# Performance work log

Measured on AMD Instinct MI355X. Metric: run time of the kernel, lower is better.

## Reference

```python
import jax, jax.numpy as jnp
import numpy as np

ALPHA = 0.0
# tetra edge vertex pairs, same order as the original: (0,1),(0,2),(0,3),(1,2),(1,3),(2,3)
EDGE_PAIRS = np.array([[0, 1], [0, 2], [0, 3], [1, 2], [1, 3], [2, 3]], dtype=np.int32)


def setup_inputs() -> dict:
    key = jax.random.key(0)
    B, N, T = 2, 120000, 600000
    k1, k2 = jax.random.split(key)
    pred = jax.random.normal(k1, (B, N, 4), dtype=jnp.float32)
    tetra = jax.random.randint(k2, (B, T, 4), 0, N, dtype=jnp.int32)
    return {"pred": pred, "tetra": tetra}


def _laplace_tetra(verts, faces):
    # verts: [N,4], faces: [T,4] int. For vertex slot j, contribution is
    # sum_{k != j} (v_k - v_j) = (v0+v1+v2+v3) - 4*v_j ; weight 3 per incidence.
    N = verts.shape[0]
    v = verts[faces]                                  # [T,4,4]
    vsum = jnp.sum(v, axis=1, keepdims=True)          # [T,1,4]
    contrib = (vsum - 4.0 * v).reshape(-1, 4)         # [T*4,4]
    idx = faces.reshape(-1)
    term = jax.ops.segment_sum(contrib, idx, num_segments=N)
    norm = jax.ops.segment_sum(jnp.full(idx.shape, 3.0, verts.dtype), idx, num_segments=N)
    term = term / jnp.clip(norm, 1.0)[:, None]
    return jnp.mean(term ** 2)


def reference(pred, tetra):
    tetra = tetra.astype(jnp.int32)
    # center pred over the point dimension (axis=1)
    pred = pred - jnp.mean(pred, axis=1, keepdims=True)

    def per_batch(pre, tetr):
        L1 = _laplace_tetra(pre, tetr)
        Tetrah = pre[tetr]                             # [T,4,4]
        pa = Tetrah[:, EDGE_PAIRS[:, 0], :]            # [T,6,4] edge endpoint 0
        pb = Tetrah[:, EDGE_PAIRS[:, 1], :]            # [T,6,4] edge endpoint 1
        wa = pa[..., 3]
        wb = pb[..., 3]
        edge = (wa - ALPHA) * (wb - ALPHA)             # [T,6]
        L2 = jnp.mean(wa * wb)
        L3 = jnp.mean((jnp.linalg.norm(pa - pb, axis=-1) - 0.4) ** 2)
        # zero-crossing interpolation: x = (alpha - w0)*m/q + x0
        d = pa - pb                                    # [T,6,4]
        q = d[..., 3]
        safe_q = jnp.where(jnp.abs(q) > 1e-12, q, 1.0)
        t = (ALPHA - wa) / safe_q                      # [T,6]
        pts = pa[..., :3] + t[..., None] * d[..., :3]  # [T,6,3]
        mask = edge < 0                                # valid crossing edges
        pts = jnp.where(mask[..., None], pts, 0.0)
        return L1, L2, L3, pts, mask

    L1, L2, L3, pts, mask = jax.vmap(per_batch)(pred, tetra)
    # losses = [L1, L2, L3, L4] (L4 is always 0 in the original)
    losses = jnp.stack([jnp.mean(L1), jnp.mean(L2), jnp.mean(L3), jnp.zeros((), pred.dtype)])
    return losses, pts, mask
```

## Files before the change

### kernel.cpp

```cpp
#include <hip/hip_runtime.h>


#define VPB 2048
#define VPB_SHIFT 11
#define KMAX 120
#define LAP_M 8
#define CAP 49152u
#define FP_BIAS 16.0f
#define FP_SCALE 8.0f
#define FP_INV   0.125f
#define FMASK 0x3FFFULL

typedef float vf4  __attribute__((ext_vector_type(4)));
typedef float vf4u __attribute__((ext_vector_type(4), aligned(4)));
typedef int   vi4  __attribute__((ext_vector_type(4)));

__device__ inline double waveReduce(double v) {
    #pragma unroll
    for (int off = 32; off > 0; off >>= 1) v += __shfl_down(v, off);
    return v;
}

__device__ inline void block_copy_nt(float* __restrict__ dst,
                                     const float* __restrict__ src, int n) {
    int n4 = n >> 2;
    const vf4* s4 = (const vf4*)src;
    vf4u* d4 = (vf4u*)dst;
    for (int i = threadIdx.x; i < n4; i += 256) {
        vf4u v = s4[i];
        __builtin_nontemporal_store(v, d4 + i);
    }
    for (int i = (n4 << 2) + threadIdx.x; i < n; i += 256)
        dst[i] = src[i];
}

__device__ inline void block_copy_u8_nt(float* __restrict__ dst,
                                        const unsigned char* __restrict__ src,
                                        int n) {
    int n4 = n >> 2;
    const uchar4* s4 = (const uchar4*)src;
    vf4u* d4 = (vf4u*)dst;
    for (int i = threadIdx.x; i < n4; i += 256) {
        uchar4 c = s4[i];
        vf4u v = { (float)c.x, (float)c.y, (float)c.z, (float)c.w };
        __builtin_nontemporal_store(v, d4 + i);
    }
    for (int i = (n4 << 2) + threadIdx.x; i < n; i += 256)
        dst[i] = (float)src[i];
}

__global__ __launch_bounds__(256) void mean_kernel(
    const float* __restrict__ pred, double* __restrict__ mpart,
    unsigned* __restrict__ cursors, int N)
{
    if (blockIdx.x == 0 && blockIdx.y == 0 && threadIdx.x < KMAX)
        cursors[threadIdx.x] = 0u;

    const int b = blockIdx.y;
    const float4* p = (const float4*)pred + (size_t)b * N;
    double s0 = 0, s1 = 0, s2 = 0, s3 = 0;
    for (int n = blockIdx.x * blockDim.x + threadIdx.x; n < N;
         n += gridDim.x * blockDim.x) {
        float4 v = p[n];
        s0 += v.x; s1 += v.y; s2 += v.z; s3 += v.w;
    }
    s0 = waveReduce(s0); s1 = waveReduce(s1);
    s2 = waveReduce(s2); s3 = waveReduce(s3);
    __shared__ double mr[4][4];
    int wv = threadIdx.x >> 6;
    if ((threadIdx.x & 63) == 0) {
        mr[wv][0] = s0; mr[wv][1] = s1; mr[wv][2] = s2; mr[wv][3] = s3;
    }
    __syncthreads();
    if (threadIdx.x < 4) {
        double a = mr[0][threadIdx.x] + mr[1][threadIdx.x]
                 + mr[2][threadIdx.x] + mr[3][threadIdx.x];
        mpart[((size_t)b * 32 + blockIdx.x) * 4 + threadIdx.x] = a;
    }
}

__device__ inline void edge_phase(const float4* vr,
                                  float m0, float m1, float m2, float m3,
                                  double& l2, double& l3,
                                  float* lds_pts, unsigned char* lds_msk)
{
    float4 v[4];
    #pragma unroll
    for (int s = 0; s < 4; s++)
        v[s] = make_float4(vr[s].x - m0, vr[s].y - m1, vr[s].z - m2, vr[s].w - m3);
    const int EA[6] = {0, 0, 0, 1, 1, 2};
    const int EB[6] = {1, 2, 3, 2, 3, 3};
    #pragma unroll
    for (int e = 0; e < 6; e++) {
        float4 pa = v[EA[e]], pb = v[EB[e]];
        float wa = pa.w, wb = pb.w;
        float edge = wa * wb;
        float dx = pa.x - pb.x, dy = pa.y - pb.y;
        float dz = pa.z - pb.z, dw = pa.w - pb.w;
        l2 += (double)edge;
        float nr = sqrtf(dx * dx + dy * dy + dz * dz + dw * dw) - 0.4f;
        l3 += (double)(nr * nr);
        float sq = (fabsf(dw) > 1e-12f) ? dw : 1.0f;
        float tt = (0.0f - wa) / sq;
        bool msk = edge < 0.0f;
        lds_pts[threadIdx.x * 18 + e * 3 + 0] = msk ? (pa.x + tt * dx) : 0.0f;
        lds_pts[threadIdx.x * 18 + e * 3 + 1] = msk ? (pa.y + tt * dy) : 0.0f;
        lds_pts[threadIdx.x * 18 + e * 3 + 2] = msk ? (pa.z + tt * dz) : 0.0f;
        lds_msk[threadIdx.x * 6 + e] = msk ? 1 : 0;
    }
}

__device__ inline unsigned long long pack_rec(const float4* vr) {
    float sx = vr[0].x + vr[1].x + vr[2].x + vr[3].x;
    float sy = vr[0].y + vr[1].y + vr[2].y + vr[3].y;
    float sz = vr[0].z + vr[1].z + vr[2].z + vr[3].z;
    float sw = vr[0].w + vr[1].w + vr[2].w + vr[3].w;
    unsigned long long qx = (unsigned long long)((sx + FP_BIAS) * FP_SCALE + 0.5f);
    unsigned long long qy = (unsigned long long)((sy + FP_BIAS) * FP_SCALE + 0.5f);
    unsigned long long qz = (unsigned long long)((sz + FP_BIAS) * FP_SCALE + 0.5f);
    unsigned long long qw = (unsigned long long)((sw + FP_BIAS) * FP_SCALE + 0.5f);
    return qx | (qy << 9) | (qz << 18) | (qw << 27);
}

__device__ inline unsigned long long pack_ab(const float4* vr) {
    float sx = vr[0].x + vr[1].x + vr[2].x + vr[3].x;
    float sy = vr[0].y + vr[1].y + vr[2].y + vr[3].y;
    float sz = vr[0].z + vr[1].z + vr[2].z + vr[3].z;
    float sw = vr[0].w + vr[1].w + vr[2].w + vr[3].w;
    unsigned long long qx = (unsigned long long)((sx + FP_BIAS) * FP_SCALE + 0.5f);
    unsigned long long qy = (unsigned long long)((sy + FP_BIAS) * FP_SCALE + 0.5f);
    unsigned long long qz = (unsigned long long)((sz + FP_BIAS) * FP_SCALE + 0.5f);
    unsigned long long qw = (unsigned long long)((sw + FP_BIAS) * FP_SCALE + 0.5f);
    return qx | (qy << 14) | (qz << 28) | (qw << 42) | (1ULL << 56);
}

__global__ __launch_bounds__(256) void fused_kernel(
    const float* __restrict__ pred, const int* __restrict__ tetra,
    const double* __restrict__ mpart,
    unsigned long long* __restrict__ seg,
    unsigned* __restrict__ cursors,
    unsigned long long* __restrict__ AB,
    double* __restrict__ l2p, double* __restrict__ l3p,
    float* __restrict__ out, int N, int T, int B, int K, int mode)
{
    __shared__ __align__(16) float lds_pts[256 * 18];
    __shared__ __align__(16) unsigned char lds_msk[256 * 6];
    __shared__ double sr[2][4];
    __shared__ unsigned hist[KMAX];
    __shared__ unsigned basei[KMAX];
    __shared__ float bm[4];

    const int b = blockIdx.y;

    if (threadIdx.x < KMAX) hist[threadIdx.x] = 0;
    if (threadIdx.x < 4) {
        double s = 0.0;
        #pragma unroll
        for (int j = 0; j < 32; j++)
            s += mpart[((size_t)b * 32 + j) * 4 + threadIdx.x];
        bm[threadIdx.x] = (float)(s / N);
    }
    __syncthreads();

    const int tbase = blockIdx.x * 512;
    const int t0 = tbase + threadIdx.x;
    const int t1 = tbase + 256 + threadIdx.x;
    const bool v0 = (t0 < T), v1 = (t1 < T);
    float m0 = bm[0], m1 = bm[1], m2 = bm[2], m3 = bm[3];

    double l2 = 0.0, l3 = 0.0;
    int via[4] = {0,0,0,0}, vib[4] = {0,0,0,0};
    unsigned rnka[4] = {0,0,0,0}, rnkb[4] = {0,0,0,0};
    float4 vra[4], vrb[4];
    unsigned long long recq0 = 0, recq1 = 0;

    if (v0) {
        vi4 q = __builtin_nontemporal_load((const vi4*)tetra + (size_t)b * T + t0);
        via[0] = q.x; via[1] = q.y; via[2] = q.z; via[3] = q.w;
        #pragma unroll
        for (int s = 0; s < 4; s++)
            vra[s] = ((const float4*)pred)[(size_t)b * N + via[s]];
    }
    if (v1) {
        vi4 q = __builtin_nontemporal_load((const vi4*)tetra + (size_t)b * T + t1);
        vib[0] = q.x; vib[1] = q.y; vib[2] = q.z; vib[3] = q.w;
        #pragma unroll
        for (int s = 0; s < 4; s++)
            vrb[s] = ((const float4*)pred)[(size_t)b * N + vib[s]];
    }

    if (mode == 1) {
        if (v0) {
            #pragma unroll
            for (int s = 0; s < 4; s++) {
                unsigned gid = (unsigned)(b * N + via[s]);
                rnka[s] = atomicAdd(&hist[gid >> VPB_SHIFT], 1u);
            }
        }
        if (v1) {
            #pragma unroll
            for (int s = 0; s < 4; s++) {
                unsigned gid = (unsigned)(b * N + vib[s]);
                rnkb[s] = atomicAdd(&hist[gid >> VPB_SHIFT], 1u);
            }
        }
    }

    if (v0) {
        recq0 = (mode == 1) ? pack_rec(vra) : pack_ab(vra);
        edge_phase(vra, m0, m1, m2, m3, l2, l3, lds_pts, lds_msk);
    }
    __syncthreads();

    if (mode == 1 && threadIdx.x < K) {
        unsigned h = hist[threadIdx.x];
        basei[threadIdx.x] = h ? atomicAdd(&cursors[threadIdx.x], h) : 0u;
    }

    const int nv0 = min(256, T - tbase);
    {
        size_t pbase = 4 + ((size_t)b * T + tbase) * 18;
        block_copy_nt(out + pbase, lds_pts, nv0 * 18);
        size_t mbase = 4 + (size_t)B * T * 18 + ((size_t)b * T + tbase) * 6;
        block_copy_u8_nt(out + mbase, lds_msk, nv0 * 6);
    }
    __syncthreads();

    if (v1) {
        recq1 = (mode == 1) ? pack_rec(vrb) : pack_ab(vrb);
        edge_phase(vrb, m0, m1, m2, m3, l2, l3, lds_pts, lds_msk);
    }
    l2 = waveReduce(l2); l3 = waveReduce(l3);
    int wv = threadIdx.x >> 6;
    if ((threadIdx.x & 63) == 0) { sr[0][wv] = l2; sr[1][wv] = l3; }
    __syncthreads();

    const int nv1 = min(256, T - tbase - 256);
    if (nv1 > 0) {
        size_t pbase = 4 + ((size_t)b * T + tbase + 256) * 18;
        block_copy_nt(out + pbase, lds_pts, nv1 * 18);
        size_t mbase = 4 + (size_t)B * T * 18 + ((size_t)b * T + tbase + 256) * 6;
        block_copy_u8_nt(out + mbase, lds_msk, nv1 * 6);
    }

    if (threadIdx.x == 0) {
        double a = 0, c = 0;
        #pragma unroll
        for (int w = 0; w < 4; w++) { a += sr[0][w]; c += sr[1][w]; }
        int blk = blockIdx.y * gridDim.x + blockIdx.x;
        l2p[blk] = a;
        l3p[blk] = c;
    }

    if (mode == 1) {
        if (v0) {
            #pragma unroll
            for (int s = 0; s < 4; s++) {
                unsigned gid = (unsigned)(b * N + via[s]);
                unsigned bk = gid >> VPB_SHIFT;
                unsigned slot = basei[bk] + rnka[s];
                if (slot < CAP)
                    seg[(size_t)bk * CAP + slot] =
                        recq0 | ((unsigned long long)(gid & (VPB - 1)) << 36);
            }
        }
        if (v1) {
            #pragma unroll
            for (int s = 0; s < 4; s++) {
                unsigned gid = (unsigned)(b * N + vib[s]);
                unsigned bk = gid >> VPB_SHIFT;
                unsigned slot = basei[bk] + rnkb[s];
                if (slot < CAP)
                    seg[(size_t)bk * CAP + slot] =
                        recq1 | ((unsigned long long)(gid & (VPB - 1)) << 36);
            }
        }
    } else {
        if (v0) {
            #pragma unroll
            for (int s = 0; s < 4; s++)
                atomicAdd(&AB[(size_t)b * N + via[s]], recq0);
        }
        if (v1) {
            #pragma unroll
            for (int s = 0; s < 4; s++)
                atomicAdd(&AB[(size_t)b * N + vib[s]], recq1);
        }
    }
}

__device__ inline unsigned long long rec_decode(unsigned long long r) {
    return (r & 511ULL)
         | (((r >> 9)  & 511ULL) << 14)
         | (((r >> 18) & 511ULL) << 28)
         | (((r >> 27) & 511ULL) << 42)
         | (1ULL << 56);
}

__global__ __launch_bounds__(256) void lap1_kernel(
    const unsigned long long* __restrict__ seg,
    const unsigned* __restrict__ cursors,
    unsigned long long* __restrict__ partial, int M)
{
    __shared__ unsigned long long acc[VPB];
    const int bkt = blockIdx.x;
    const int m = blockIdx.y;

    for (int i = threadIdx.x; i < VPB; i += 256) acc[i] = 0ULL;
    __syncthreads();

    unsigned cnt = min(cursors[bkt], CAP);
    unsigned per = (cnt + M - 1) / M;
    unsigned lo = m * per;
    unsigned hi = min(cnt, lo + per);
    const unsigned long long* s0 = seg + (size_t)bkt * CAP;

    unsigned i = lo + threadIdx.x;
    for (; i + 768 < hi; i += 1024) {
        unsigned long long r0 = __builtin_nontemporal_load(&s0[i]);
        unsigned long long r1 = __builtin_nontemporal_load(&s0[i + 256]);
        unsigned long long r2 = __builtin_nontemporal_load(&s0[i + 512]);
        unsigned long long r3 = __builtin_nontemporal_load(&s0[i + 768]);
        atomicAdd(&acc[(unsigned)(r0 >> 36) & (VPB - 1)], rec_decode(r0));
        atomicAdd(&acc[(unsigned)(r1 >> 36) & (VPB - 1)], rec_decode(r1));
        atomicAdd(&acc[(unsigned)(r2 >> 36) & (VPB - 1)], rec_decode(r2));
        atomicAdd(&acc[(unsigned)(r3 >> 36) & (VPB - 1)], rec_decode(r3));
    }
    for (; i < hi; i += 256) {
        unsigned long long r = __builtin_nontemporal_load(&s0[i]);
        atomicAdd(&acc[(unsigned)(r >> 36) & (VPB - 1)], rec_decode(r));
    }
    __syncthreads();

    unsigned long long* p = partial + ((size_t)bkt * M + m) * VPB;
    for (int i2 = threadIdx.x; i2 < VPB; i2 += 256) p[i2] = acc[i2];
}

__global__ __launch_bounds__(256) void lap2_kernel(
    const unsigned long long* __restrict__ partial,
    const float* __restrict__ pred, double* __restrict__ l1p, int BN, int M)
{
    int gid = blockIdx.x * 256 + threadIdx.x;
    double s = 0.0;
    if (gid < BN) {
        int bkt = gid >> VPB_SHIFT;
        int rel = gid & (VPB - 1);
        const unsigned long long* p =
            partial + (size_t)bkt * M * VPB + rel;
        unsigned long long P = 0;
        #pragma unroll 4
        for (int m = 0; m < M; m++) P += p[(size_t)m * VPB];
        int c = (int)(P >> 56);
        float cb = (float)c * FP_BIAS;
        float Sx = (float)(unsigned)( P        & FMASK) * FP_INV - cb;
        float Sy = (float)(unsigned)((P >> 14) & FMASK) * FP_INV - cb;
        float Sz = (float)(unsigned)((P >> 28) & FMASK) * FP_INV - cb;
        float Sw = (float)(unsigned)((P >> 42) & FMASK) * FP_INV - cb;
        float4 v = ((const float4*)pred)[gid];
        float fc = 4.0f * (float)c;
        float tx = Sx - fc * v.x, ty = Sy - fc * v.y;
        float tz = Sz - fc * v.z, tw = Sw - fc * v.w;
        float dn = fmaxf(3.0f * (float)c, 1.0f);
        tx /= dn; ty /= dn; tz /= dn; tw /= dn;
        s = (double)(tx * tx) + (double)(ty * ty)
          + (double)(tz * tz) + (double)(tw * tw);
    }
    s = waveReduce(s);
    __shared__ double sr[4];
    int wv = threadIdx.x >> 6;
    if ((threadIdx.x & 63) == 0) sr[wv] = s;
    __syncthreads();
    if (threadIdx.x == 0) {
        double a = 0;
        #pragma unroll
        for (int w = 0; w < 4; w++) a += sr[w];
        l1p[blockIdx.x] = a;
    }
}

__global__ __launch_bounds__(256) void l1_kernel(
    const unsigned long long* __restrict__ AB, const float* __restrict__ pred,
    double* __restrict__ l1p, int BN)
{
    int i = blockIdx.x * 256 + threadIdx.x;
    double s = 0.0;
    if (i < BN) {
        unsigned long long P = AB[i];
        int c = (int)(P >> 56);
        float cb = (float)c * FP_BIAS;
        float Sx = (float)(unsigned)( P        & FMASK) * FP_INV - cb;
        float Sy = (float)(unsigned)((P >> 14) & FMASK) * FP_INV - cb;
        float Sz = (float)(unsigned)((P >> 28) & FMASK) * FP_INV - cb;
        float Sw = (float)(unsigned)((P >> 42) & FMASK) * FP_INV - cb;
        float4 v = ((const float4*)pred)[i];
        float fc = 4.0f * (float)c;
        float tx = Sx - fc * v.x, ty = Sy - fc * v.y;
        float tz = Sz - fc * v.z, tw = Sw - fc * v.w;
        float dn = fmaxf(3.0f * (float)c, 1.0f);
        tx /= dn; ty /= dn; tz /= dn; tw /= dn;
        s = (double)(tx * tx) + (double)(ty * ty)
          + (double)(tz * tz) + (double)(tw * tw);
    }
    s = waveReduce(s);
    __shared__ double sr[4];
    int wv = threadIdx.x >> 6;
    if ((threadIdx.x & 63) == 0) sr[wv] = s;
    __syncthreads();
    if (threadIdx.x == 0) {
        double a = 0;
        #pragma unroll
        for (int w = 0; w < 4; w++) a += sr[w];
        l1p[blockIdx.x] = a;
    }
}

__global__ __launch_bounds__(256) void finalize_kernel(
    const double* __restrict__ l1p, const double* __restrict__ l2p,
    const double* __restrict__ l3p, float* __restrict__ out,
    double nd1, double nd23, int n1, int n23)
{
    double s1 = 0, s2 = 0, s3 = 0;
    for (int i = threadIdx.x; i < n23; i += 256) { s2 += l2p[i]; s3 += l3p[i]; }
    for (int i = threadIdx.x; i < n1; i += 256) s1 += l1p[i];
    s1 = waveReduce(s1); s2 = waveReduce(s2); s3 = waveReduce(s3);
    __shared__ double sr[3][4];
    int wv = threadIdx.x >> 6;
    if ((threadIdx.x & 63) == 0) { sr[0][wv] = s1; sr[1][wv] = s2; sr[2][wv] = s3; }
    __syncthreads();
    if (threadIdx.x == 0) {
        double a = 0, b = 0, c = 0;
        #pragma unroll
        for (int w = 0; w < 4; w++) { a += sr[0][w]; b += sr[1][w]; c += sr[2][w]; }
        out[0] = (float)(a / nd1);
        out[1] = (float)(b / nd23);
        out[2] = (float)(c / nd23);
        out[3] = 0.0f;
    }
}

extern "C" void kernel_launch(void* const* d_in, const int* in_sizes, int n_in,
                              void* d_out, int out_size, void* d_ws, size_t ws_size,
                              hipStream_t stream) {
    const float* pred = (const float*)d_in[0];
    const int* tetra = (const int*)d_in[1];
    float* out = (float*)d_out;

    const int B = 2;
    const int N = in_sizes[0] / (B * 4);
    const int T = in_sizes[1] / (B * 4);
    const int BN = B * N;
    const int K = (BN + VPB - 1) >> VPB_SHIFT;

    char* ws = (char*)d_ws;
    double* mpart = (double*)ws;
    unsigned* cursors = (unsigned*)(ws + 2048);
    double* l1p = (double*)(ws + 2560);
    double* l2p = (double*)(ws + 68096);
    double* l3p = (double*)(ws + 133632);
    char* dyn = ws + 199168;

    size_t seg_bytes = (size_t)K * CAP * 8;
    int M = 0;
    if ((K <= KMAX) &&
        ws_size >= 199168 + seg_bytes + (size_t)K * LAP_M * VPB * 8) M = LAP_M;

    dim3 mg(32, B);
    dim3 tg((T + 511) / 512, B);
    const int n23 = B * ((T + 511) / 512);
    const int nvb = (BN + 255) / 256;
    double nd1 = (double)BN * 4.0;
    double nd23 = (double)B * (double)T * 6.0;

    if (M > 0) {
        unsigned long long* seg = (unsigned long long*)dyn;
        unsigned long long* partial = (unsigned long long*)(dyn + seg_bytes);
        mean_kernel<<<mg, 256, 0, stream>>>(pred, mpart, cursors, N);
        fused_kernel<<<tg, 256, 0, stream>>>(pred, tetra, mpart, seg, cursors,
                                             nullptr, l2p, l3p, out,
                                             N, T, B, K, 1);
        dim3 lg(K, M);
        lap1_kernel<<<lg, 256, 0, stream>>>(seg, cursors, partial, M);
        lap2_kernel<<<nvb, 256, 0, stream>>>(partial, pred, l1p, BN, M);
        finalize_kernel<<<1, 256, 0, stream>>>(l1p, l2p, l3p, out,
                                               nd1, nd23, nvb, n23);
    } else {
        unsigned long long* AB = (unsigned long long*)dyn;
        (void)hipMemsetAsync(dyn, 0, (size_t)BN * 8, stream);
        mean_kernel<<<mg, 256, 0, stream>>>(pred, mpart, cursors, N);
        fused_kernel<<<tg, 256, 0, stream>>>(pred, tetra, mpart, nullptr, cursors,
                                             AB, l2p, l3p, out,
                                             N, T, B, K, 0);
        l1_kernel<<<nvb, 256, 0, stream>>>(AB, pred, l1p, BN);
        finalize_kernel<<<1, 256, 0, stream>>>(l1p, l2p, l3p, out,
                                               nd1, nd23, nvb, n23);
    }
}
```

Baseline: 217.6 us.

## Fuse bucket accumulation and L1 reduction into one 1024-thread kernel per bucket

Replaces the two-kernel Laplacian path with a single kernel. Previously each bucket was split across M blocks that wrote partial accumulators to global memory, and a second kernel summed them. Now one 1024-thread block per bucket accumulates all records into shared memory and computes the L1 term directly. This removes the partial-buffer write/read and one launch, but cuts the grid from K*8 blocks to K blocks (about 118), so fewer blocks are available to fill the GPU.

```diff
diff --git a/kernel.cpp b/kernel.cpp
--- a/kernel.cpp
+++ b/kernel.cpp
@@ -4,7 +4,6 @@
 #define VPB 2048
 #define VPB_SHIFT 11
 #define KMAX 120
-#define LAP_M 8
 #define CAP 49152u
 #define FP_BIAS 16.0f
 #define FP_SCALE 8.0f
@@ -297,84 +296,70 @@
          | (1ULL << 56);
 }
 
-__global__ __launch_bounds__(256) void lap1_kernel(
+__global__ __launch_bounds__(1024) void biglap_kernel(
     const unsigned long long* __restrict__ seg,
     const unsigned* __restrict__ cursors,
-    unsigned long long* __restrict__ partial, int M)
+    const float* __restrict__ pred, double* __restrict__ l1p, int BN)
 {
     __shared__ unsigned long long acc[VPB];
+    __shared__ double sr[16];
     const int bkt = blockIdx.x;
-    const int m = blockIdx.y;
-
-    for (int i = threadIdx.x; i < VPB; i += 256) acc[i] = 0ULL;
+    const int tid = threadIdx.x;
+
+    for (int i = tid; i < VPB; i += 1024) acc[i] = 0ULL;
     __syncthreads();
 
     unsigned cnt = min(cursors[bkt], CAP);
-    unsigned per = (cnt + M - 1) / M;
-    unsigned lo = m * per;
-    unsigned hi = min(cnt, lo + per);
     const unsigned long long* s0 = seg + (size_t)bkt * CAP;
 
-    unsigned i = lo + threadIdx.x;
-    for (; i + 768 < hi; i += 1024) {
+    unsigned i = tid;
+    for (; i + 3072 < cnt; i += 4096) {
         unsigned long long r0 = __builtin_nontemporal_load(&s0[i]);
-        unsigned long long r1 = __builtin_nontemporal_load(&s0[i + 256]);
-        unsigned long long r2 = __builtin_nontemporal_load(&s0[i + 512]);
-        unsigned long long r3 = __builtin_nontemporal_load(&s0[i + 768]);
+        unsigned long long r1 = __builtin_nontemporal_load(&s0[i + 1024]);
+        unsigned long long r2 = __builtin_nontemporal_load(&s0[i + 2048]);
+        unsigned long long r3 = __builtin_nontemporal_load(&s0[i + 3072]);
         atomicAdd(&acc[(unsigned)(r0 >> 36) & (VPB - 1)], rec_decode(r0));
         atomicAdd(&acc[(unsigned)(r1 >> 36) & (VPB - 1)], rec_decode(r1));
         atomicAdd(&acc[(unsigned)(r2 >> 36) & (VPB - 1)], rec_decode(r2));
         atomicAdd(&acc[(unsigned)(r3 >> 36) & (VPB - 1)], rec_decode(r3));
     }
-    for (; i < hi; i += 256) {
+    for (; i < cnt; i += 1024) {
         unsigned long long r = __builtin_nontemporal_load(&s0[i]);
         atomicAdd(&acc[(unsigned)(r >> 36) & (VPB - 1)], rec_decode(r));
     }
     __syncthreads();
 
-    unsigned long long* p = partial + ((size_t)bkt * M + m) * VPB;
-    for (int i2 = threadIdx.x; i2 < VPB; i2 += 256) p[i2] = acc[i2];
-}
-
-__global__ __launch_bounds__(256) void lap2_kernel(
-    const unsigned long long* __restrict__ partial,
-    const float* __restrict__ pred, double* __restrict__ l1p, int BN, int M)
-{
-    int gid = blockIdx.x * 256 + threadIdx.x;
+    const int base = bkt << VPB_SHIFT;
     double s = 0.0;
-    if (gid < BN) {
-        int bkt = gid >> VPB_SHIFT;
-        int rel = gid & (VPB - 1);
-        const unsigned long long* p =
-            partial + (size_t)bkt * M * VPB + rel;
-        unsigned long long P = 0;
-        #pragma unroll 4
-        for (int m = 0; m < M; m++) P += p[(size_t)m * VPB];
-        int c = (int)(P >> 56);
-        float cb = (float)c * FP_BIAS;
-        float Sx = (float)(unsigned)( P        & FMASK) * FP_INV - cb;
-        float Sy = (float)(unsigned)((P >> 14) & FMASK) * FP_INV - cb;
-        float Sz = (float)(unsigned)((P >> 28) & FMASK) * FP_INV - cb;
-        float Sw = (float)(unsigned)((P >> 42) & FMASK) * FP_INV - cb;
-        float4 v = ((const float4*)pred)[gid];
-        float fc = 4.0f * (float)c;
-        float tx = Sx - fc * v.x, ty = Sy - fc * v.y;
-        float tz = Sz - fc * v.z, tw = Sw - fc * v.w;
-        float dn = fmaxf(3.0f * (float)c, 1.0f);
-        tx /= dn; ty /= dn; tz /= dn; tw /= dn;
-        s = (double)(tx * tx) + (double)(ty * ty)
-          + (double)(tz * tz) + (double)(tw * tw);
+    for (int v = tid; v < VPB; v += 1024) {
+        int gid = base + v;
+        if (gid < BN) {
+            unsigned long long P = acc[v];
+            int c = (int)(P >> 56);
+            float cb = (float)c * FP_BIAS;
+            float Sx = (float)(unsigned)( P        & FMASK) * FP_INV - cb;
+            float Sy = (float)(unsigned)((P >> 14) & FMASK) * FP_INV - cb;
+            float Sz = (float)(unsigned)((P >> 28) & FMASK) * FP_INV - cb;
+            float Sw = (float)(unsigned)((P >> 42) & FMASK) * FP_INV - cb;
+            float4 v4 = ((const float4*)pred)[gid];
+            float fc = 4.0f * (float)c;
+            float tx = Sx - fc * v4.x, ty = Sy - fc * v4.y;
+            float tz = Sz - fc * v4.z, tw = Sw - fc * v4.w;
+            float dn = fmaxf(3.0f * (float)c, 1.0f);
+            tx /= dn; ty /= dn; tz /= dn; tw /= dn;
+            s += (double)(tx * tx) + (double)(ty * ty)
+               + (double)(tz * tz) + (double)(tw * tw);
+        }
     }
     s = waveReduce(s);
-    __shared__ double sr[4];
-    int wv = threadIdx.x >> 6;
-    if ((threadIdx.x & 63) == 0) sr[wv] = s;
-    __syncthreads();
-    if (threadIdx.x == 0) {
+    int wv = tid >> 6;
+    if ((tid & 63) == 0) sr[wv] = s;
+    __syncthreads();
+    if (tid == 0) {
         double a = 0;
         #pragma unroll
-        for (int w = 0; w < 4; w++) a += sr[w];
-        l1p[blockIdx.x] = a;
+        for (int w = 0; w < 16; w++) a += sr[w];
+        l1p[bkt] = a;
     }
 }
 
@@ -460,9 +445,7 @@
     char* dyn = ws + 199168;
 
     size_t seg_bytes = (size_t)K * CAP * 8;
-    int M = 0;
-    if ((K <= KMAX) &&
-        ws_size >= 199168 + seg_bytes + (size_t)K * LAP_M * VPB * 8) M = LAP_M;
+    bool rec = (K <= KMAX) && (ws_size >= 199168 + seg_bytes);
 
     dim3 mg(32, B);
     dim3 tg((T + 511) / 512, B);
@@ -471,18 +454,15 @@
     double nd1 = (double)BN * 4.0;
     double nd23 = (double)B * (double)T * 6.0;
 
-    if (M > 0) {
+    if (rec) {
         unsigned long long* seg = (unsigned long long*)dyn;
-        unsigned long long* partial = (unsigned long long*)(dyn + seg_bytes);
         mean_kernel<<<mg, 256, 0, stream>>>(pred, mpart, cursors, N);
         fused_kernel<<<tg, 256, 0, stream>>>(pred, tetra, mpart, seg, cursors,
                                              nullptr, l2p, l3p, out,
                                              N, T, B, K, 1);
-        dim3 lg(K, M);
-        lap1_kernel<<<lg, 256, 0, stream>>>(seg, cursors, partial, M);
-        lap2_kernel<<<nvb, 256, 0, stream>>>(partial, pred, l1p, BN, M);
+        biglap_kernel<<<K, 1024, 0, stream>>>(seg, cursors, pred, l1p, BN);
         finalize_kernel<<<1, 256, 0, stream>>>(l1p, l2p, l3p, out,
-                                               nd1, nd23, nvb, n23);
+                                               nd1, nd23, K, n23);
     } else {
         unsigned long long* AB = (unsigned long long*)dyn;
         (void)hipMemsetAsync(dyn, 0, (size_t)BN * 8, stream);
```

Result: faster. 209.5 us (-3.7%).
